# Kernel tuning notes

Hardware: AMD Instinct MI355X
Metric: run time of the kernel (lower is better)

## Reference

```python
import jax, jax.numpy as jnp
import numpy as np
import math

B, LA, LB, D, H = 8, 2048, 2048, 512, 512

def setup_inputs() -> dict:
    key = jax.random.key(0)
    ks = jax.random.split(key, 6)
    return {
        "input_a": jax.random.normal(ks[0], (B, LA, D), dtype=jnp.float32),
        "input_b": jax.random.normal(ks[1], (B, LB, D), dtype=jnp.float32),
        "mask_a": jax.random.randint(ks[2], (B, LA), 0, 2, dtype=jnp.int32),
        "mask_b": jax.random.randint(ks[3], (B, LB), 0, 2, dtype=jnp.int32),
        "Wa": jax.random.normal(ks[4], (D, H), dtype=jnp.float32) * (1.0 / math.sqrt(D)),
        "ba": jnp.zeros((H,), dtype=jnp.float32),
        "Wb": jax.random.normal(ks[5], (D, H), dtype=jnp.float32) * (1.0 / math.sqrt(D)),
        "bb": jnp.zeros((H,), dtype=jnp.float32),
    }

def reference(input_a, input_b, mask_a, mask_b, Wa, ba, Wb, bb):
    scale = 1.0 / math.sqrt(D)  # math.sqrt(input_dim_a)
    mapped_a = input_a @ Wa + ba            # [B, La, H]
    mapped_b = input_b @ Wb + bb            # [B, Lb, H]
    # final_mask = (mask_a outer mask_b) == 0
    final_mask = (mask_a[:, :, None] * mask_b[:, None, :]) == 0  # [B, La, Lb]
    scores = jnp.einsum('bih,bjh->bij', mapped_a, mapped_b) * scale
    scores = jnp.where(final_mask, jnp.float32(-1e9), scores)
    # attentions_a = softmax over Lb; attentions_b^T = softmax over La axis
    att_a = jax.nn.softmax(scores, axis=-1)   # [B, La, Lb]
    att_bT = jax.nn.softmax(scores, axis=1)   # [B, La, Lb] (= attentions_b.transpose(1,2))
    output_a = jnp.einsum('bij,bjd->bid', att_bT, input_b)  # [B, La, D]
    output_b = jnp.einsum('bij,bid->bjd', att_a, input_a)   # [B, Lb, D]
    return (output_a + input_a, output_b + input_b)
```

## Files before the change

kernel.cpp:

```cpp
#include <hip/hip_runtime.h>
#include <hip/hip_bf16.h>

#define BATCH 8
#define LSEQ 2048
#define DDIM 512

using f32x4 = __attribute__((ext_vector_type(4))) float;
using s16x8 = __attribute__((ext_vector_type(8))) short;

static __device__ __forceinline__ unsigned short f2b(float f) {
  __hip_bfloat16 h = __float2bfloat16(f);
  return __builtin_bit_cast(unsigned short, h);
}
static __device__ __forceinline__ float b2f(unsigned short u) {
  unsigned int v = ((unsigned int)u) << 16;
  return __builtin_bit_cast(float, v);
}

static __device__ __forceinline__ void gld16(const unsigned short* g, unsigned short* l) {
  __builtin_amdgcn_global_load_lds(
      (__attribute__((address_space(1))) void*)(g),
      (__attribute__((address_space(3))) void*)(l), 16, 0, 0);
}

__device__ __forceinline__ void mfma_kloop(
    const unsigned short* __restrict__ A, const unsigned short* __restrict__ Bt,
    int K, int lda, int ldb, unsigned short* sA, unsigned short* sB,
    int tid, f32x4 acc[4][4]) {
  const int wave = tid >> 6, lane = tid & 63;
  const int wm = (wave >> 1) * 64, wn = (wave & 1) * 64;
  const int lr = lane & 15, lq = lane >> 4;
  const int srow = tid >> 2;
  const int sk = (tid & 3) * 8;
  unsigned short* dA0 = sA + wave * 512;
  unsigned short* dA1 = sA + 2048 + wave * 512;
  unsigned short* dB0 = sB + wave * 512;
  unsigned short* dB1 = sB + 2048 + wave * 512;
  const unsigned short* pa0 = A + (size_t)srow * lda + sk;
  const unsigned short* pa1 = A + (size_t)(srow + 64) * lda + sk;
  const unsigned short* pb0 = Bt + (size_t)srow * ldb + sk;
  const unsigned short* pb1 = Bt + (size_t)(srow + 64) * ldb + sk;
  for (int k0 = 0; k0 < K; k0 += 32) {
    gld16(pa0 + k0, dA0);
    gld16(pa1 + k0, dA1);
    gld16(pb0 + k0, dB0);
    gld16(pb1 + k0, dB1);
    __syncthreads();
    s16x8 af[4], bf[4];
#pragma unroll
    for (int r = 0; r < 4; ++r)
      af[r] = *(const s16x8*)(sA + (wm + r * 16 + lr) * 32 + lq * 8);
#pragma unroll
    for (int c = 0; c < 4; ++c)
      bf[c] = *(const s16x8*)(sB + (wn + c * 16 + lr) * 32 + lq * 8);
#pragma unroll
    for (int r = 0; r < 4; ++r)
#pragma unroll
      for (int c = 0; c < 4; ++c)
        acc[r][c] = __builtin_amdgcn_mfma_f32_16x16x32_bf16(af[r], bf[c], acc[r][c], 0, 0, 0);
    __syncthreads();
  }
}

__global__ __launch_bounds__(256) void k_prep(const float* __restrict__ in_a,
                                              const float* __restrict__ in_b,
                                              const int* __restrict__ ma,
                                              const int* __restrict__ mb,
                                              unsigned short* __restrict__ oa,
                                              unsigned short* __restrict__ ob,
                                              float* __restrict__ Pa,
                                              float* __restrict__ Pb) {
  int z = blockIdx.z;
  const float* in = z ? in_b : in_a;
  const int* mask = z ? mb : ma;
  unsigned short* o16 = z ? ob : oa;
  float* partial = z ? Pb : Pa;
  int b = blockIdx.y;
  int l0 = blockIdx.x * 32;
  __shared__ int sm[32];
  if (threadIdx.x < 32) sm[threadIdx.x] = mask[b * LSEQ + l0 + threadIdx.x];
  __syncthreads();
  int d = threadIdx.x * 2;
  const float* base = in + ((size_t)b * LSEQ + l0) * DDIM + d;
  unsigned short* obase = o16 + ((size_t)b * LSEQ + l0) * DDIM + d;
  float ax = 0.f, ay = 0.f;
#pragma unroll 4
  for (int r = 0; r < 32; ++r) {
    float2 v = *(const float2*)(base + (size_t)r * DDIM);
    ushort2 u; u.x = f2b(v.x); u.y = f2b(v.y);
    *(ushort2*)(obase + (size_t)r * DDIM) = u;
    if (sm[r] == 0) { ax += v.x; ay += v.y; }
  }
  float2 o; o.x = ax; o.y = ay;
  *(float2*)(partial + ((size_t)(b * 64 + blockIdx.x)) * DDIM + d) = o;
}

__global__ __launch_bounds__(256) void k_p2(const float* __restrict__ Pa,
                                            const float* __restrict__ Pb,
                                            float* __restrict__ Ca,
                                            float* __restrict__ Cb) {
  int g = blockIdx.x;
  const float* src = (g < 8) ? Pa : Pb;
  float* dst = (g < 8) ? Ca : Cb;
  int b = g & 7;
  int d = threadIdx.x * 2;
  float ax = 0.f, ay = 0.f;
  for (int c = 0; c < 64; ++c) {
    float2 v = *(const float2*)(src + ((size_t)(b * 64 + c)) * DDIM + d);
    ax += v.x; ay += v.y;
  }
  dst[b * DDIM + d] = ax * (1.0f / LSEQ);
  dst[b * DDIM + d + 1] = ay * (1.0f / LSEQ);
}

__global__ __launch_bounds__(256) void k_transposeW(const float* __restrict__ Wa,
                                                    const float* __restrict__ Wb,
                                                    unsigned short* __restrict__ WaT,
                                                    unsigned short* __restrict__ WbT) {
  int gidx = blockIdx.x * 256 + threadIdx.x;
  const float* W = (gidx < 512 * 512) ? Wa : Wb;
  unsigned short* WT = (gidx < 512 * 512) ? WaT : WbT;
  int idx = gidx & (512 * 512 - 1);
  int h = idx >> 9, d = idx & 511;
  WT[idx] = f2b(W[d * DDIM + h]);
}

__global__ __launch_bounds__(256) void k_gemm_bias(const unsigned short* __restrict__ a16,
                                                   const unsigned short* __restrict__ b16,
                                                   const unsigned short* __restrict__ WaT,
                                                   const unsigned short* __restrict__ WbT,
                                                   const float* __restrict__ ba,
                                                   const float* __restrict__ bb,
                                                   unsigned short* __restrict__ mapa,
                                                   unsigned short* __restrict__ mapb) {
  int z = blockIdx.z;
  const unsigned short* A = z ? b16 : a16;
  const unsigned short* Bt = z ? WbT : WaT;
  const float* bias = z ? bb : ba;
  unsigned short* Cout = z ? mapb : mapa;
  __shared__ __align__(16) unsigned short sA[128 * 32], sB[128 * 32];
  f32x4 acc[4][4];
  f32x4 zero = {0.f, 0.f, 0.f, 0.f};
#pragma unroll
  for (int r = 0; r < 4; ++r)
#pragma unroll
    for (int c = 0; c < 4; ++c) acc[r][c] = zero;
  int bm = blockIdx.y * 128, bn = blockIdx.x * 128;
  mfma_kloop(A + (size_t)bm * DDIM, Bt + (size_t)bn * DDIM, DDIM, DDIM, DDIM,
             sA, sB, threadIdx.x, acc);
  int wave = threadIdx.x >> 6, lane = threadIdx.x & 63;
  int wm = (wave >> 1) * 64, wn = (wave & 1) * 64, lr = lane & 15, lq = lane >> 4;
#pragma unroll
  for (int r = 0; r < 4; ++r)
#pragma unroll
    for (int c = 0; c < 4; ++c)
#pragma unroll
      for (int rr = 0; rr < 4; ++rr) {
        int row = bm + wm + r * 16 + lq * 4 + rr;
        int col = bn + wn + c * 16 + lr;
        Cout[(size_t)row * DDIM + col] = f2b(acc[r][c][rr] + bias[col]);
      }
}

__global__ __launch_bounds__(256) void k_scores(const unsigned short* __restrict__ mapa,
                                                const unsigned short* __restrict__ mapb,
                                                const int* __restrict__ mask_a,
                                                const int* __restrict__ mask_b,
                                                unsigned short* __restrict__ E,
                                                float* __restrict__ Zrow,
                                                float* __restrict__ Zcol) {
  __shared__ __align__(16) unsigned short sA[128 * 32], sB[128 * 32];
  __shared__ int sMa[128], sMb[128];
  int b = blockIdx.z;
  int bi = blockIdx.y * 128, bj = blockIdx.x * 128;
  int tid = threadIdx.x;
  if (tid < 128)
    sMa[tid] = mask_a[b * LSEQ + bi + tid];
  else
    sMb[tid - 128] = mask_b[b * LSEQ + bj + tid - 128];
  f32x4 acc[4][4];
  f32x4 zero = {0.f, 0.f, 0.f, 0.f};
#pragma unroll
  for (int r = 0; r < 4; ++r)
#pragma unroll
    for (int c = 0; c < 4; ++c) acc[r][c] = zero;
  mfma_kloop(mapa + ((size_t)b * LSEQ + bi) * DDIM, mapb + ((size_t)b * LSEQ + bj) * DDIM,
             DDIM, DDIM, DDIM, sA, sB, tid, acc);
  const float scale = 0.044194173824159216f;
  int wave = tid >> 6, lane = tid & 63;
  int wm = (wave >> 1) * 64, wn = (wave & 1) * 64, lr = lane & 15, lq = lane >> 4;
  unsigned short* Eb = E + (size_t)b * LSEQ * LSEQ + (size_t)bi * LSEQ + bj;
  float colp[4] = {0.f, 0.f, 0.f, 0.f};
  float rowp[4][4];
#pragma unroll
  for (int r = 0; r < 4; ++r) {
#pragma unroll
    for (int rr = 0; rr < 4; ++rr) rowp[r][rr] = 0.f;
#pragma unroll
    for (int c = 0; c < 4; ++c) {
      int jl = wn + c * 16 + lr;
      int mb_ = sMb[jl];
#pragma unroll
      for (int rr = 0; rr < 4; ++rr) {
        int il = wm + r * 16 + lq * 4 + rr;
        float e = (sMa[il] && mb_) ? __expf(acc[r][c][rr] * scale) : 0.f;
        rowp[r][rr] += e;
        colp[c] += e;
        Eb[(size_t)il * LSEQ + jl] = f2b(e);
      }
    }
  }
#pragma unroll
  for (int r = 0; r < 4; ++r)
#pragma unroll
    for (int rr = 0; rr < 4; ++rr) {
      float v = rowp[r][rr];
      v += __shfl_xor(v, 1);
      v += __shfl_xor(v, 2);
      v += __shfl_xor(v, 4);
      v += __shfl_xor(v, 8);
      if (lr == 0) {
        int il = wm + r * 16 + lq * 4 + rr;
        atomicAdd(&Zrow[b * LSEQ + bi + il], v);
      }
    }
#pragma unroll
  for (int c = 0; c < 4; ++c) {
    float v = colp[c];
    v += __shfl_xor(v, 16);
    v += __shfl_xor(v, 32);
    if (lq == 0) atomicAdd(&Zcol[b * LSEQ + bj + wn + c * 16 + lr], v);
  }
}

__global__ __launch_bounds__(256) void k_scaleT(const unsigned short* __restrict__ a16,
                                                const unsigned short* __restrict__ b16,
                                                const float* __restrict__ Zrow,
                                                const float* __restrict__ Zcol,
                                                unsigned short* __restrict__ atS,
                                                unsigned short* __restrict__ btS) {
  int zz = blockIdx.z;
  int b = zz & 7, sel = zz >> 3;
  const unsigned short* in = sel ? b16 : a16;
  const float* Z = sel ? Zcol : Zrow;
  unsigned short* out = sel ? btS : atS;
  int i0 = blockIdx.y * 64, d0 = blockIdx.x * 64;
  __shared__ unsigned short lt[64 * 65];
  __shared__ float zinv[64];
  if (threadIdx.x < 64) {
    float z = Z[b * LSEQ + i0 + threadIdx.x];
    zinv[threadIdx.x] = (z > 0.f) ? 1.f / z : 0.f;
  }
  __syncthreads();
  const unsigned short* ib = in + ((size_t)b * LSEQ + i0) * DDIM + d0;
#pragma unroll
  for (int p = 0; p < 16; ++p) {
    int idx = p * 256 + threadIdx.x;
    int dl = idx & 63, il = idx >> 6;
    lt[dl * 65 + il] = f2b(b2f(ib[(size_t)il * DDIM + dl]) * zinv[il]);
  }
  __syncthreads();
  unsigned short* ob = out + ((size_t)b * DDIM + d0) * LSEQ + i0;
#pragma unroll
  for (int p = 0; p < 16; ++p) {
    int idx = p * 256 + threadIdx.x;
    int il = idx & 63, dl = idx >> 6;
    ob[(size_t)dl * LSEQ + il] = lt[dl * 65 + il];
  }
}

__global__ __launch_bounds__(256) void k_gemm_out(const unsigned short* __restrict__ Eop,
                                                  const unsigned short* __restrict__ Sop,
                                                  const float* __restrict__ addin,
                                                  const float* __restrict__ Cvec,
                                                  float* __restrict__ Out) {
  __shared__ __align__(16) unsigned short sA[128 * 32], sB[128 * 32];
  int b = blockIdx.z;
  int bm = blockIdx.y * 128, bn = blockIdx.x * 128;
  f32x4 acc[4][4];
  f32x4 zero = {0.f, 0.f, 0.f, 0.f};
#pragma unroll
  for (int r = 0; r < 4; ++r)
#pragma unroll
    for (int c = 0; c < 4; ++c) acc[r][c] = zero;
  mfma_kloop(Eop + (size_t)b * LSEQ * LSEQ + (size_t)bm * LSEQ,
             Sop + (size_t)b * DDIM * LSEQ + (size_t)bn * LSEQ,
             LSEQ, LSEQ, LSEQ, sA, sB, threadIdx.x, acc);
  int wave = threadIdx.x >> 6, lane = threadIdx.x & 63;
  int wm = (wave >> 1) * 64, wn = (wave & 1) * 64, lr = lane & 15, lq = lane >> 4;
#pragma unroll
  for (int r = 0; r < 4; ++r)
#pragma unroll
    for (int c = 0; c < 4; ++c)
#pragma unroll
      for (int rr = 0; rr < 4; ++rr) {
        int row = bm + wm + r * 16 + lq * 4 + rr;
        int col = bn + wn + c * 16 + lr;
        size_t o = ((size_t)b * LSEQ + row) * DDIM + col;
        Out[o] = acc[r][c][rr] + addin[o] + Cvec[b * DDIM + col];
      }
}

__global__ __launch_bounds__(256) void k_gemm_outT(const unsigned short* __restrict__ E,
                                                   const unsigned short* __restrict__ Sop,
                                                   const float* __restrict__ addin,
                                                   const float* __restrict__ Cvec,
                                                   float* __restrict__ Out) {
  __shared__ __align__(16) unsigned short sA[128 * 32], sB[128 * 32];
  int b = blockIdx.z;
  int bm = blockIdx.y * 128, bn = blockIdx.x * 128;
  int tid = threadIdx.x;
  const int wave = tid >> 6, lane = tid & 63;
  const int wm = (wave >> 1) * 64, wn = (wave & 1) * 64;
  const int lr = lane & 15, lq = lane >> 4;
  const int srow = tid >> 2, sk = (tid & 3) * 8;
  f32x4 acc[4][4];
  f32x4 zero = {0.f, 0.f, 0.f, 0.f};
#pragma unroll
  for (int r = 0; r < 4; ++r)
#pragma unroll
    for (int c = 0; c < 4; ++c) acc[r][c] = zero;
  unsigned short* dB0 = sB + wave * 512;
  unsigned short* dB1 = sB + 2048 + wave * 512;
  const unsigned short* Bb = Sop + (size_t)b * DDIM * LSEQ + (size_t)bn * LSEQ;
  const unsigned short* pb0 = Bb + (size_t)srow * LSEQ + sk;
  const unsigned short* pb1 = Bb + (size_t)(srow + 64) * LSEQ + sk;
  const int tk = (tid & 15) * 2;
  const int tm = (tid >> 4) * 8;
  const unsigned short* pe = E + (size_t)b * LSEQ * LSEQ + (size_t)tk * LSEQ + bm + tm;
  for (int k0 = 0; k0 < LSEQ; k0 += 32) {
    gld16(pb0 + k0, dB0);
    gld16(pb1 + k0, dB1);
    uint4 e0 = *(const uint4*)(pe + (size_t)k0 * LSEQ);
    uint4 e1 = *(const uint4*)(pe + (size_t)k0 * LSEQ + LSEQ);
    unsigned short t0[8], t1[8];
    *(uint4*)t0 = e0; *(uint4*)t1 = e1;
#pragma unroll
    for (int j = 0; j < 8; ++j) {
      unsigned int v = (unsigned int)t0[j] | ((unsigned int)t1[j] << 16);
      *(unsigned int*)(sA + (tm + j) * 32 + tk) = v;
    }
    __syncthreads();
    s16x8 af[4], bf[4];
#pragma unroll
    for (int r = 0; r < 4; ++r)
      af[r] = *(const s16x8*)(sA + (wm + r * 16 + lr) * 32 + lq * 8);
#pragma unroll
    for (int c = 0; c < 4; ++c)
      bf[c] = *(const s16x8*)(sB + (wn + c * 16 + lr) * 32 + lq * 8);
#pragma unroll
    for (int r = 0; r < 4; ++r)
#pragma unroll
      for (int c = 0; c < 4; ++c)
        acc[r][c] = __builtin_amdgcn_mfma_f32_16x16x32_bf16(af[r], bf[c], acc[r][c], 0, 0, 0);
    __syncthreads();
  }
#pragma unroll
  for (int r = 0; r < 4; ++r)
#pragma unroll
    for (int c = 0; c < 4; ++c)
#pragma unroll
      for (int rr = 0; rr < 4; ++rr) {
        int row = bm + wm + r * 16 + lq * 4 + rr;
        int col = bn + wn + c * 16 + lr;
        size_t o = ((size_t)b * LSEQ + row) * DDIM + col;
        Out[o] = acc[r][c][rr] + addin[o] + Cvec[b * DDIM + col];
      }
}

extern "C" void kernel_launch(void* const* d_in, const int* in_sizes, int n_in,
                              void* d_out, int out_size, void* d_ws, size_t ws_size,
                              hipStream_t stream) {
  (void)in_sizes; (void)n_in; (void)out_size; (void)ws_size;
  const float* in_a = (const float*)d_in[0];
  const float* in_b = (const float*)d_in[1];
  const int* ma = (const int*)d_in[2];
  const int* mb = (const int*)d_in[3];
  const float* Wa = (const float*)d_in[4];
  const float* ba = (const float*)d_in[5];
  const float* Wb = (const float*)d_in[6];
  const float* bb = (const float*)d_in[7];
  float* out = (float*)d_out;

  char* ws = (char*)d_ws;
  const size_t MB = 1ull << 20;
  unsigned short* a16 = (unsigned short*)(ws + 0 * MB);
  unsigned short* b16 = (unsigned short*)(ws + 16 * MB);
  unsigned short* WaT = (unsigned short*)(ws + 32 * MB);
  unsigned short* WbT = (unsigned short*)(ws + 32 * MB + 512 * 1024);
  unsigned short* mapa = (unsigned short*)(ws + 33 * MB);
  unsigned short* mapb = (unsigned short*)(ws + 49 * MB);
  unsigned short* E = (unsigned short*)(ws + 65 * MB);
  unsigned short* atS = (unsigned short*)(ws + 129 * MB);
  unsigned short* btS = (unsigned short*)(ws + 145 * MB);
  float* Zrow = (float*)(ws + 161 * MB);
  float* Zcol = (float*)(ws + 161 * MB + 65536);
  float* Ca = (float*)(ws + 161 * MB + 2 * 65536);
  float* Cb = (float*)(ws + 161 * MB + 2 * 65536 + 16384);
  float* Pa = (float*)(ws + 162 * MB);
  float* Pb = (float*)(ws + 163 * MB);

  hipMemsetAsync(Zrow, 0, 2 * 65536, stream);
  k_prep<<<dim3(64, 8, 2), 256, 0, stream>>>(in_a, in_b, ma, mb, a16, b16, Pa, Pb);
  k_transposeW<<<2048, 256, 0, stream>>>(Wa, Wb, WaT, WbT);
  k_p2<<<16, 256, 0, stream>>>(Pa, Pb, Ca, Cb);
  k_gemm_bias<<<dim3(4, 128, 2), 256, 0, stream>>>(a16, b16, WaT, WbT, ba, bb, mapa, mapb);
  k_scores<<<dim3(16, 16, 8), 256, 0, stream>>>(mapa, mapb, ma, mb, E, Zrow, Zcol);
  k_scaleT<<<dim3(8, 32, 16), 256, 0, stream>>>(a16, b16, Zrow, Zcol, atS, btS);
  k_gemm_out<<<dim3(4, 16, 8), 256, 0, stream>>>(E, btS, in_a, Cb, out);
  k_gemm_outT<<<dim3(4, 16, 8), 256, 0, stream>>>(E, atS, in_b, Ca,
                                                  out + (size_t)BATCH * LSEQ * DDIM);
}
```

Before: 382.6 us.

## Remap GEMM block indices for XCD-aware locality and swizzle transposed LDS tile

Flattens the launch grids of four GEMM kernels to 1D and remaps block IDs so that groups of eight consecutive blocks (likely landing on different XCDs with round-robin dispatch) share input tiles within each XCD's L2. Blocks on the same die then reuse rows and columns in cache. Separately, the transposed-write path in k_gemm_outT gets an XOR swizzle on the LDS A tile to reduce bank conflicts on both the scatter writes and the fragment reads. The cost is extra index arithmetic, and the approach depends on the hardware's block-to-XCD dispatch order.

```diff
diff --git a/kernel.cpp b/kernel.cpp
--- a/kernel.cpp
+++ b/kernel.cpp
@@ -133,7 +133,12 @@
                                                    const float* __restrict__ bb,
                                                    unsigned short* __restrict__ mapa,
                                                    unsigned short* __restrict__ mapb) {
-  int z = blockIdx.z;
+  int id = blockIdx.x;
+  int g = id >> 5, rem = id & 31;
+  int bn = (rem >> 3) * 128;
+  int f = g * 8 + (rem & 7);
+  int bm = (f & 127) * 128;
+  int z = f >> 7;
   const unsigned short* A = z ? b16 : a16;
   const unsigned short* Bt = z ? WbT : WaT;
   const float* bias = z ? bb : ba;
@@ -145,7 +150,6 @@
   for (int r = 0; r < 4; ++r)
 #pragma unroll
     for (int c = 0; c < 4; ++c) acc[r][c] = zero;
-  int bm = blockIdx.y * 128, bn = blockIdx.x * 128;
   mfma_kloop(A + (size_t)bm * DDIM, Bt + (size_t)bn * DDIM, DDIM, DDIM, DDIM,
              sA, sB, threadIdx.x, acc);
   int wave = threadIdx.x >> 6, lane = threadIdx.x & 63;
@@ -169,10 +173,15 @@
                                                 unsigned short* __restrict__ E,
                                                 float* __restrict__ Zrow,
                                                 float* __restrict__ Zcol) {
+  int id = blockIdx.x;
+  int low = id & 7, rest = id >> 3;
+  int sub = rest & 15, Ghi = rest >> 4;
+  int G = Ghi * 8 + low;
+  int b = G >> 4, super = G & 15;
+  int bi = (((super >> 2) << 2) + (sub >> 2)) * 128;
+  int bj = (((super & 3) << 2) + (sub & 3)) * 128;
   __shared__ __align__(16) unsigned short sA[128 * 32], sB[128 * 32];
   __shared__ int sMa[128], sMb[128];
-  int b = blockIdx.z;
-  int bi = blockIdx.y * 128, bj = blockIdx.x * 128;
   int tid = threadIdx.x;
   if (tid < 128)
     sMa[tid] = mask_a[b * LSEQ + bi + tid];
@@ -274,9 +283,13 @@
                                                   const float* __restrict__ addin,
                                                   const float* __restrict__ Cvec,
                                                   float* __restrict__ Out) {
+  int id = blockIdx.x;
+  int g = id >> 5, rem = id & 31;
+  int bn = (rem >> 3) * 128;
+  int f = g * 8 + (rem & 7);
+  int bm = (f & 15) * 128;
+  int b = f >> 4;
   __shared__ __align__(16) unsigned short sA[128 * 32], sB[128 * 32];
-  int b = blockIdx.z;
-  int bm = blockIdx.y * 128, bn = blockIdx.x * 128;
   f32x4 acc[4][4];
   f32x4 zero = {0.f, 0.f, 0.f, 0.f};
 #pragma unroll
@@ -306,9 +319,13 @@
                                                    const float* __restrict__ addin,
                                                    const float* __restrict__ Cvec,
                                                    float* __restrict__ Out) {
+  int id = blockIdx.x;
+  int g = id >> 5, rem = id & 31;
+  int bn = (rem >> 3) * 128;
+  int f = g * 8 + (rem & 7);
+  int bm = (f & 15) * 128;
+  int b = f >> 4;
   __shared__ __align__(16) unsigned short sA[128 * 32], sB[128 * 32];
-  int b = blockIdx.z;
-  int bm = blockIdx.y * 128, bn = blockIdx.x * 128;
   int tid = threadIdx.x;
   const int wave = tid >> 6, lane = tid & 63;
   const int wm = (wave >> 1) * 64, wn = (wave & 1) * 64;
@@ -325,8 +342,10 @@
   const unsigned short* Bb = Sop + (size_t)b * DDIM * LSEQ + (size_t)bn * LSEQ;
   const unsigned short* pb0 = Bb + (size_t)srow * LSEQ + sk;
   const unsigned short* pb1 = Bb + (size_t)(srow + 64) * LSEQ + sk;
-  const int tk = (tid & 15) * 2;
+  const int tc = tid & 15;
+  const int tk = tc * 2;
   const int tm = (tid >> 4) * 8;
+  const int gq = tc >> 2, wq = tc & 3;
   const unsigned short* pe = E + (size_t)b * LSEQ * LSEQ + (size_t)tk * LSEQ + bm + tm;
   for (int k0 = 0; k0 < LSEQ; k0 += 32) {
     gld16(pb0 + k0, dB0);
@@ -337,14 +356,18 @@
     *(uint4*)t0 = e0; *(uint4*)t1 = e1;
 #pragma unroll
     for (int j = 0; j < 8; ++j) {
+      int row = tm + j;
+      int sw = gq ^ ((row >> 3) & 3);
       unsigned int v = (unsigned int)t0[j] | ((unsigned int)t1[j] << 16);
-      *(unsigned int*)(sA + (tm + j) * 32 + tk) = v;
+      *(unsigned int*)(sA + row * 32 + sw * 8 + wq * 2) = v;
     }
     __syncthreads();
     s16x8 af[4], bf[4];
 #pragma unroll
-    for (int r = 0; r < 4; ++r)
-      af[r] = *(const s16x8*)(sA + (wm + r * 16 + lr) * 32 + lq * 8);
+    for (int r = 0; r < 4; ++r) {
+      int R = wm + r * 16 + lr;
+      af[r] = *(const s16x8*)(sA + R * 32 + ((lq ^ ((R >> 3) & 3)) * 8));
+    }
 #pragma unroll
     for (int c = 0; c < 4; ++c)
       bf[c] = *(const s16x8*)(sB + (wn + c * 16 + lr) * 32 + lq * 8);
@@ -404,10 +427,10 @@
   k_prep<<<dim3(64, 8, 2), 256, 0, stream>>>(in_a, in_b, ma, mb, a16, b16, Pa, Pb);
   k_transposeW<<<2048, 256, 0, stream>>>(Wa, Wb, WaT, WbT);
   k_p2<<<16, 256, 0, stream>>>(Pa, Pb, Ca, Cb);
-  k_gemm_bias<<<dim3(4, 128, 2), 256, 0, stream>>>(a16, b16, WaT, WbT, ba, bb, mapa, mapb);
-  k_scores<<<dim3(16, 16, 8), 256, 0, stream>>>(mapa, mapb, ma, mb, E, Zrow, Zcol);
+  k_gemm_bias<<<1024, 256, 0, stream>>>(a16, b16, WaT, WbT, ba, bb, mapa, mapb);
+  k_scores<<<2048, 256, 0, stream>>>(mapa, mapb, ma, mb, E, Zrow, Zcol);
   k_scaleT<<<dim3(8, 32, 16), 256, 0, stream>>>(a16, b16, Zrow, Zcol, atS, btS);
-  k_gemm_out<<<dim3(4, 16, 8), 256, 0, stream>>>(E, btS, in_a, Cb, out);
-  k_gemm_outT<<<dim3(4, 16, 8), 256, 0, stream>>>(E, atS, in_b, Ca,
-                                                  out + (size_t)BATCH * LSEQ * DDIM);
-}
+  k_gemm_out<<<512, 256, 0, stream>>>(E, btS, in_a, Cb, out);
+  k_gemm_outT<<<512, 256, 0, stream>>>(E, atS, in_b, Ca,
+                                       out + (size_t)BATCH * LSEQ * DDIM);
+}
```

New measurement: 378.3 us. No clear change (-1.1%).
